# Optimization experiments

Measured on AMD Instinct MI355X. Metric: run time of the kernel, lower is better.

## Reference

```python
import jax, jax.numpy as jnp
import numpy as np

N_NODES = 100000
N_EDGES = 1600000
IN_DIM = 128
OUT_DIM = 128
NEG_SLOPE = 0.2


def setup_inputs() -> dict:
    key = jax.random.key(0)
    ks = jax.random.split(key, 7)
    x = jax.random.normal(ks[0], (N_NODES, IN_DIM), dtype=jnp.float32)
    edge_index = jax.random.randint(ks[1], (2, N_EDGES), 0, N_NODES, dtype=jnp.int32)
    # xavier-ish scale for [in, out] weight layout (y = x @ W)
    s = float(np.sqrt(2.0 / (IN_DIM + OUT_DIM)))
    W_q = jax.random.normal(ks[2], (IN_DIM, OUT_DIM), dtype=jnp.float32) * s
    W_k = jax.random.normal(ks[3], (IN_DIM, OUT_DIM), dtype=jnp.float32) * s
    W_v = jax.random.normal(ks[4], (IN_DIM, OUT_DIM), dtype=jnp.float32) * s
    W_l = jax.random.normal(ks[5], (IN_DIM, OUT_DIM), dtype=jnp.float32) * s
    b_l = jnp.zeros((OUT_DIM,), dtype=jnp.float32)
    return {"x": x, "edge_index": edge_index, "W_q": W_q, "W_k": W_k,
            "W_v": W_v, "W_l": W_l, "b_l": b_l}


def reference(x, edge_index, W_q, W_k, W_v, W_l, b_l):
    num_nodes = x.shape[0]
    row, col = edge_index[0], edge_index[1]

    h_q = x @ W_q                                   # [N, D]
    h_k = x @ W_k                                   # [N, D]
    _h_v = x @ W_v                                  # computed in original, unused downstream

    # aggregated query: sum of neighbor queries per destination node
    q_agg = jax.ops.segment_sum(h_q[col], row, num_segments=num_nodes)  # [N, D]
    k_act = jax.nn.leaky_relu(h_k, NEG_SLOPE)

    # per-edge attention scores (note: original uses raw q_agg, not activated)
    scores = jnp.sum(k_act[row] * q_agg[col], axis=1) / (OUT_DIM ** 0.5)  # [E]

    # scatter-softmax over edges grouped by destination (row)
    max_val = jax.ops.segment_max(scores, row, num_segments=num_nodes)
    exp_scores = jnp.exp(scores - max_val[row])
    sum_exp = jax.ops.segment_sum(exp_scores, row, num_segments=num_nodes)
    alpha = exp_scores / (sum_exp[row] + 1e-8)      # [E]; dropout is identity in eval

    h_proj = x @ W_l + b_l                          # [N, D]
    weighted = alpha[:, None] * h_proj[col]         # [E, D]
    h_prime = jax.ops.segment_sum(weighted, row, num_segments=num_nodes)
    return jax.nn.leaky_relu(h_prime, NEG_SLOPE)
```

## Files before the change

kernel.cpp:

```cpp
#include <hip/hip_runtime.h>
#include <math.h>

#define N_NODES 100000
#define N_EDGES 1600000
#define DIM 128
#define CAP 64

#define NB1 196
#define NPB 512
#define CHUNK1 4096
#define GRID1 391
#define SLOT1 52
#define LSTRIDE 197

typedef short bf16x8 __attribute__((ext_vector_type(8)));
typedef float f32x4 __attribute__((ext_vector_type(4)));

static __device__ __forceinline__ unsigned bf16rne(float f) {
    unsigned u = __float_as_uint(f);
    return (u + 0x7FFFu + ((u >> 16) & 1u)) >> 16;
}
static __device__ __forceinline__ float bflo(unsigned u) { return __uint_as_float(u << 16); }
static __device__ __forceinline__ float bfhi(unsigned u) { return __uint_as_float(u & 0xFFFF0000u); }


__global__ __launch_bounds__(256) void prep_k(
    const float* __restrict__ x, const float* __restrict__ Wq,
    const float* __restrict__ Wk, const float* __restrict__ Wl,
    ushort* __restrict__ xb, ushort* __restrict__ kactb,
    ushort* __restrict__ WqTh, ushort* __restrict__ WqTl,
    ushort* __restrict__ WlTh, ushort* __restrict__ WlTl) {
    __shared__ ushort bh[128 * 136];
    __shared__ ushort blo[128 * 136];
    int t = threadIdx.x;

    if (blockIdx.x < 2) {
        const float* W = (blockIdx.x == 0) ? Wq : Wl;
        ushort* Th = (blockIdx.x == 0) ? WqTh : WlTh;
        ushort* Tl = (blockIdx.x == 0) ? WqTl : WlTl;
        for (int i = t; i < 16384; i += 256) {
            int k = i >> 7, n = i & 127;
            float v = W[i];
            unsigned hi = bf16rne(v);
            float lo = v - bflo(hi);
            Th[n * 128 + k] = (ushort)hi;
            Tl[n * 128 + k] = (ushort)bf16rne(lo);
        }
    }
    for (int i = t; i < 16384; i += 256) {
        int k = i >> 7, n = i & 127;
        float v = Wk[i];
        unsigned hi = bf16rne(v);
        float lo = v - bflo(hi);
        bh[n * 136 + k] = (ushort)hi;
        blo[n * 136 + k] = (ushort)bf16rne(lo);
    }
    __syncthreads();

    int wave = t >> 6, lane = t & 63;
    int ln15 = lane & 15, quad = lane >> 4;
    long base = (long)blockIdx.x * 128 + wave * 32;

    bf16x8 Af[2][4];
#pragma unroll
    for (int r = 0; r < 2; r++) {
        long row = base + r * 16 + ln15;
        long rowc = row < N_NODES ? row : N_NODES - 1;
#pragma unroll
        for (int s = 0; s < 4; s++) {
            int ch = s * 4 + quad;
            const float4* xp = (const float4*)(x + rowc * 128 + ch * 8);
            float4 u0 = xp[0], u1 = xp[1];
            bf16x8 f;
            f[0] = (short)bf16rne(u0.x); f[1] = (short)bf16rne(u0.y);
            f[2] = (short)bf16rne(u0.z); f[3] = (short)bf16rne(u0.w);
            f[4] = (short)bf16rne(u1.x); f[5] = (short)bf16rne(u1.y);
            f[6] = (short)bf16rne(u1.z); f[7] = (short)bf16rne(u1.w);
            Af[r][s] = f;
            if (row < N_NODES) *(bf16x8*)(xb + row * 128 + ch * 8) = f;
        }
    }
    f32x4 acc[2][8];
#pragma unroll
    for (int r = 0; r < 2; r++)
#pragma unroll
        for (int t8 = 0; t8 < 8; t8++) acc[r][t8] = (f32x4){0.f, 0.f, 0.f, 0.f};
#pragma unroll
    for (int phase = 0; phase < 2; phase++) {
        const ushort* B = phase ? blo : bh;
#pragma unroll
        for (int s = 0; s < 4; s++) {
#pragma unroll
            for (int t8 = 0; t8 < 8; t8++) {
                bf16x8 b = *(const bf16x8*)(B + (t8 * 16 + ln15) * 136 + (s * 4 + quad) * 8);
                acc[0][t8] = __builtin_amdgcn_mfma_f32_16x16x32_bf16(Af[0][s], b, acc[0][t8], 0, 0, 0);
                acc[1][t8] = __builtin_amdgcn_mfma_f32_16x16x32_bf16(Af[1][s], b, acc[1][t8], 0, 0, 0);
            }
        }
    }
#pragma unroll
    for (int r = 0; r < 2; r++) {
#pragma unroll
        for (int reg = 0; reg < 4; reg++) {
            long node = base + r * 16 + quad * 4 + reg;
            if (node < N_NODES) {
#pragma unroll
                for (int t8 = 0; t8 < 8; t8++) {
                    float v = acc[r][t8][reg];
                    v = v > 0.f ? v : 0.2f * v;
                    kactb[node * 128 + t8 * 16 + ln15] = (ushort)bf16rne(v);
                }
            }
        }
    }
}


__global__ __launch_bounds__(256) void bin_k(const int* __restrict__ row,
                                             const int* __restrict__ col,
                                             unsigned* __restrict__ bkt,
                                             int* __restrict__ bktc) {
    __shared__ int lcnt[NB1];
    __shared__ unsigned lbuf[SLOT1 * LSTRIDE];
    int t = threadIdx.x, blk = blockIdx.x;
    if (t < NB1) lcnt[t] = 0;
    __syncthreads();
    long base = (long)blk * CHUNK1;
    if (base + CHUNK1 <= N_EDGES) {
        const uint4* r4 = (const uint4*)row + (size_t)blk * 1024;
        const uint4* c4 = (const uint4*)col + (size_t)blk * 1024;
#pragma unroll
        for (int q = 0; q < 4; q++) {
            uint4 rv = r4[q * 256 + t];
            uint4 cv = c4[q * 256 + t];
            unsigned rr[4] = {rv.x, rv.y, rv.z, rv.w};
            unsigned cc[4] = {cv.x, cv.y, cv.z, cv.w};
#pragma unroll
            for (int i = 0; i < 4; i++) {
                int b = rr[i] >> 9;
                int p = atomicAdd(&lcnt[b], 1);
                if (p < SLOT1) lbuf[p * LSTRIDE + b] = (cc[i] << 9) | (rr[i] & 511u);
            }
        }
    } else {
        for (int i = t; base + i < N_EDGES; i += 256) {
            unsigned r = (unsigned)row[base + i], c = (unsigned)col[base + i];
            int b = r >> 9;
            int p = atomicAdd(&lcnt[b], 1);
            if (p < SLOT1) lbuf[p * LSTRIDE + b] = (c << 9) | (r & 511u);
        }
    }
    __syncthreads();
    if (t < NB1) bktc[(size_t)blk * NB1 + t] = min(lcnt[t], SLOT1);
    int wave = t >> 6, lane = t & 63;
    for (int s = wave; s < NB1; s += 4) {
        if (lane < min(lcnt[s], SLOT1))
            bkt[((size_t)s * GRID1 + blk) * SLOT1 + lane] = lbuf[lane * LSTRIDE + s];
    }
}


__global__ __launch_bounds__(1024) void build_k(const int* __restrict__ bktc,
                                                const unsigned* __restrict__ bkt,
                                                int* __restrict__ cur,
                                                int* __restrict__ scol) {
    __shared__ int lcur[NPB];
    __shared__ int lc[GRID1];
    int b = blockIdx.x, t = threadIdx.x;
    if (t < NPB) lcur[t] = 0;
    if (t < GRID1) lc[t] = bktc[(size_t)t * NB1 + b];
    __syncthreads();
    int wave = t >> 6, lane = t & 63;
    const unsigned* D = bkt + (size_t)b * GRID1 * SLOT1;
    for (int s = wave; s < GRID1; s += 16) {
        if (lane < lc[s]) {
            unsigned v = D[(size_t)s * SLOT1 + lane];
            int rl = (int)(v & 511u);
            int c = (int)(v >> 9);
            int p = atomicAdd(&lcur[rl], 1);
            if (p < CAP) scol[((size_t)b * NPB + rl) * CAP + p] = c;
        }
    }
    __syncthreads();
    if (t < NPB) {
        int node = b * NPB + t;
        if (node < N_NODES) cur[node] = lcur[t];
    }
}


__global__ __launch_bounds__(1024) void xq_k(const uint4* __restrict__ xb4,
                                             const int* __restrict__ cur,
                                             const int* __restrict__ scol,
                                             const ushort* __restrict__ BTh,
                                             const ushort* __restrict__ BTl,
                                             ushort* __restrict__ qb) {
    __shared__ ushort lxa[64][136];
    int t = threadIdx.x;
    int g16 = t >> 4, gl = t & 15;
    long node = (long)blockIdx.x * 64 + g16;
    int d = (node < N_NODES) ? min(cur[node], CAP) : 0;
    float a0 = 0.f, a1 = 0.f, a2 = 0.f, a3 = 0.f;
    float a4 = 0.f, a5 = 0.f, a6 = 0.f, a7 = 0.f;
    for (int j = 0; j < d; j += 16) {
        int cb = (j + gl < d) ? scol[node * CAP + j + gl] : 0;
        int lim = min(16, d - j);
        int k = 0;
        for (; k + 4 <= lim; k += 4) {
            int c0 = __shfl(cb, k, 16),     c1 = __shfl(cb, k + 1, 16);
            int c2 = __shfl(cb, k + 2, 16), c3 = __shfl(cb, k + 3, 16);
            uint4 u0 = xb4[(size_t)c0 * 16 + gl];
            uint4 u1 = xb4[(size_t)c1 * 16 + gl];
            uint4 u2 = xb4[(size_t)c2 * 16 + gl];
            uint4 u3 = xb4[(size_t)c3 * 16 + gl];
            a0 += bflo(u0.x); a1 += bfhi(u0.x); a2 += bflo(u0.y); a3 += bfhi(u0.y);
            a4 += bflo(u0.z); a5 += bfhi(u0.z); a6 += bflo(u0.w); a7 += bfhi(u0.w);
            a0 += bflo(u1.x); a1 += bfhi(u1.x); a2 += bflo(u1.y); a3 += bfhi(u1.y);
            a4 += bflo(u1.z); a5 += bfhi(u1.z); a6 += bflo(u1.w); a7 += bfhi(u1.w);
            a0 += bflo(u2.x); a1 += bfhi(u2.x); a2 += bflo(u2.y); a3 += bfhi(u2.y);
            a4 += bflo(u2.z); a5 += bfhi(u2.z); a6 += bflo(u2.w); a7 += bfhi(u2.w);
            a0 += bflo(u3.x); a1 += bfhi(u3.x); a2 += bflo(u3.y); a3 += bfhi(u3.y);
            a4 += bflo(u3.z); a5 += bfhi(u3.z); a6 += bflo(u3.w); a7 += bfhi(u3.w);
        }
        for (; k < lim; k++) {
            int c = __shfl(cb, k, 16);
            uint4 u = xb4[(size_t)c * 16 + gl];
            a0 += bflo(u.x); a1 += bfhi(u.x); a2 += bflo(u.y); a3 += bfhi(u.y);
            a4 += bflo(u.z); a5 += bfhi(u.z); a6 += bflo(u.w); a7 += bfhi(u.w);
        }
    }
    uint4 o;
    o.x = bf16rne(a0) | (bf16rne(a1) << 16);
    o.y = bf16rne(a2) | (bf16rne(a3) << 16);
    o.z = bf16rne(a4) | (bf16rne(a5) << 16);
    o.w = bf16rne(a6) | (bf16rne(a7) << 16);
    *(uint4*)&lxa[g16][gl * 8] = o;
    __syncthreads();

    int wave = t >> 6, lane = t & 63;
    int ln15 = lane & 15, quad = (lane >> 4) & 3;
    const bf16x8* Bh8 = (const bf16x8*)BTh;
    const bf16x8* Bl8 = (const bf16x8*)BTl;
#pragma unroll
    for (int ti = 0; ti < 2; ti++) {
        int T = wave + ti * 16;
        int rt = T & 3, ct = T >> 2;
        bf16x8 af[4];
#pragma unroll
        for (int s = 0; s < 4; s++)
            af[s] = *(const bf16x8*)&lxa[rt * 16 + ln15][(s * 4 + quad) * 8];
        f32x4 acc = (f32x4){0.f, 0.f, 0.f, 0.f};
#pragma unroll
        for (int phase = 0; phase < 2; phase++) {
            const bf16x8* B8 = phase ? Bl8 : Bh8;
#pragma unroll
            for (int s = 0; s < 4; s++)
                acc = __builtin_amdgcn_mfma_f32_16x16x32_bf16(
                    af[s], B8[(ct * 16 + ln15) * 16 + s * 4 + quad], acc, 0, 0, 0);
        }
#pragma unroll
        for (int reg = 0; reg < 4; reg++) {
            long n2 = (long)blockIdx.x * 64 + rt * 16 + quad * 4 + reg;
            if (n2 < N_NODES) qb[n2 * 128 + ct * 16 + ln15] = (ushort)bf16rne(acc[reg]);
        }
    }
}


__global__ __launch_bounds__(1024) void attf_k(const uint2* __restrict__ kactb2,
                                               const uint2* __restrict__ qb2,
                                               const uint2* __restrict__ xb2,
                                               const int* __restrict__ cur,
                                               const int* __restrict__ scol,
                                               const ushort* __restrict__ BTh,
                                               const ushort* __restrict__ BTl,
                                               const float* __restrict__ bl,
                                               float* __restrict__ out) {
    __shared__ ushort lxw[32][136];
    __shared__ float lsw[32];
    int t = threadIdx.x;
    int n32 = t >> 5, lane = t & 31;
    long g = (long)blockIdx.x * 32 + n32;
    int d = min(cur[g], CAP);
    uint2 ku = kactb2[g * 32 + lane];
    const float scale = 0.08838834764831845f;
    float k0 = bflo(ku.x) * scale, k1 = bfhi(ku.x) * scale;
    float k2 = bflo(ku.y) * scale, k3 = bfhi(ku.y) * scale;

    float S = 0.f;
    float a0 = 0.f, a1 = 0.f, a2 = 0.f, a3 = 0.f;
    for (int j = 0; j < d; j += 32) {
        int cb = (j + lane < d) ? scol[g * CAP + j + lane] : 0;
        int lim = min(32, d - j);
        int k = 0;
        for (; k + 4 <= lim; k += 4) {
            int c0 = __shfl(cb, k, 32),     c1 = __shfl(cb, k + 1, 32);
            int c2 = __shfl(cb, k + 2, 32), c3 = __shfl(cb, k + 3, 32);
            uint2 q0 = qb2[(size_t)c0 * 32 + lane], x0 = xb2[(size_t)c0 * 32 + lane];
            uint2 q1 = qb2[(size_t)c1 * 32 + lane], x1 = xb2[(size_t)c1 * 32 + lane];
            uint2 q2 = qb2[(size_t)c2 * 32 + lane], x2 = xb2[(size_t)c2 * 32 + lane];
            uint2 q3 = qb2[(size_t)c3 * 32 + lane], x3 = xb2[(size_t)c3 * 32 + lane];
            float p0 = k0 * bflo(q0.x) + k1 * bfhi(q0.x) + k2 * bflo(q0.y) + k3 * bfhi(q0.y);
            float p1 = k0 * bflo(q1.x) + k1 * bfhi(q1.x) + k2 * bflo(q1.y) + k3 * bfhi(q1.y);
            float p2 = k0 * bflo(q2.x) + k1 * bfhi(q2.x) + k2 * bflo(q2.y) + k3 * bfhi(q2.y);
            float p3 = k0 * bflo(q3.x) + k1 * bfhi(q3.x) + k2 * bflo(q3.y) + k3 * bfhi(q3.y);
#pragma unroll
            for (int off = 16; off > 0; off >>= 1) {
                p0 += __shfl_xor(p0, off, 32); p1 += __shfl_xor(p1, off, 32);
                p2 += __shfl_xor(p2, off, 32); p3 += __shfl_xor(p3, off, 32);
            }
            float e0 = __expf(p0), e1 = __expf(p1);
            float e2 = __expf(p2), e3 = __expf(p3);
            S += (e0 + e1) + (e2 + e3);
            a0 += e0 * bflo(x0.x) + e1 * bflo(x1.x) + e2 * bflo(x2.x) + e3 * bflo(x3.x);
            a1 += e0 * bfhi(x0.x) + e1 * bfhi(x1.x) + e2 * bfhi(x2.x) + e3 * bfhi(x3.x);
            a2 += e0 * bflo(x0.y) + e1 * bflo(x1.y) + e2 * bflo(x2.y) + e3 * bflo(x3.y);
            a3 += e0 * bfhi(x0.y) + e1 * bfhi(x1.y) + e2 * bfhi(x2.y) + e3 * bfhi(x3.y);
        }
        for (; k < lim; k++) {
            int c = __shfl(cb, k, 32);
            uint2 q = qb2[(size_t)c * 32 + lane], xx = xb2[(size_t)c * 32 + lane];
            float p = k0 * bflo(q.x) + k1 * bfhi(q.x) + k2 * bflo(q.y) + k3 * bfhi(q.y);
#pragma unroll
            for (int off = 16; off > 0; off >>= 1) p += __shfl_xor(p, off, 32);
            float e0 = __expf(p);
            S += e0;
            a0 += e0 * bflo(xx.x);
            a1 += e0 * bfhi(xx.x);
            a2 += e0 * bflo(xx.y);
            a3 += e0 * bfhi(xx.y);
        }
    }
    float inv = 1.f / (S + 1e-8f);
    uint2 o;
    o.x = bf16rne(a0 * inv) | (bf16rne(a1 * inv) << 16);
    o.y = bf16rne(a2 * inv) | (bf16rne(a3 * inv) << 16);
    *(uint2*)&lxw[n32][lane * 4] = o;
    if (lane == 0) lsw[n32] = S * inv;
    __syncthreads();

    int wave = t >> 6, l64 = t & 63;
    int ln15 = l64 & 15, quad = (l64 >> 4) & 3;
    int rt = wave & 1, ct = wave >> 1;
    const bf16x8* Bh8 = (const bf16x8*)BTh;
    const bf16x8* Bl8 = (const bf16x8*)BTl;
    bf16x8 af[4];
#pragma unroll
    for (int s = 0; s < 4; s++)
        af[s] = *(const bf16x8*)&lxw[rt * 16 + ln15][(s * 4 + quad) * 8];
    f32x4 acc = (f32x4){0.f, 0.f, 0.f, 0.f};
#pragma unroll
    for (int phase = 0; phase < 2; phase++) {
        const bf16x8* B8 = phase ? Bl8 : Bh8;
#pragma unroll
        for (int s = 0; s < 4; s++)
            acc = __builtin_amdgcn_mfma_f32_16x16x32_bf16(
                af[s], B8[(ct * 16 + ln15) * 16 + s * 4 + quad], acc, 0, 0, 0);
    }
    float blv = bl[ct * 16 + ln15];
#pragma unroll
    for (int reg = 0; reg < 4; reg++) {
        int rrow = rt * 16 + quad * 4 + reg;
        long node = (long)blockIdx.x * 32 + rrow;
        float v = acc[reg] + lsw[rrow] * blv;
        v = v > 0.f ? v : 0.2f * v;
        out[node * 128 + ct * 16 + ln15] = v;
    }
}


extern "C" void kernel_launch(void* const* d_in, const int* in_sizes, int n_in,
                              void* d_out, int out_size, void* d_ws, size_t ws_size,
                              hipStream_t stream) {
    const float* x  = (const float*)d_in[0];
    const int* row  = (const int*)d_in[1];
    const int* col  = row + N_EDGES;
    const float* Wq = (const float*)d_in[2];
    const float* Wk = (const float*)d_in[3];
    const float* Wl = (const float*)d_in[5];
    const float* bl = (const float*)d_in[6];
    float* out = (float*)d_out;

    ushort* xb    = (ushort*)d_ws;
    ushort* qb    = xb + (size_t)N_NODES * DIM;
    ushort* kactb = qb + (size_t)N_NODES * DIM;
    ushort* wbuf  = kactb + (size_t)N_NODES * DIM;
    ushort* WqTh = wbuf,             *WqTl = wbuf + 16384;
    ushort* WlTh = wbuf + 2 * 16384, *WlTl = wbuf + 3 * 16384;
    int* cur  = (int*)(wbuf + 4 * 16384);
    int* scol = cur + N_NODES;
    unsigned* bkt = (unsigned*)(scol + (size_t)N_NODES * CAP);
    int* bktc = (int*)(bkt + (size_t)NB1 * GRID1 * SLOT1);

    prep_k<<<782, 256, 0, stream>>>(x, Wq, Wk, Wl, xb, kactb,
                                    WqTh, WqTl, WlTh, WlTl);
    bin_k<<<GRID1, 256, 0, stream>>>(row, col, bkt, bktc);
    build_k<<<NB1, 1024, 0, stream>>>(bktc, bkt, cur, scol);
    xq_k<<<(N_NODES + 63) / 64, 1024, 0, stream>>>((const uint4*)xb, cur, scol,
                                                   WqTh, WqTl, qb);
    attf_k<<<N_NODES / 32, 1024, 0, stream>>>((const uint2*)kactb, (const uint2*)qb,
                                              (const uint2*)xb, cur, scol,
                                              WlTh, WlTl, bl, out);
}
```

Measured before the change: 470.3 us.

## Interleave q and x rows into one buffer and shrink attention blocks to 8 nodes

The q-projection kernel now stages its bf16 output in shared memory and writes an interleaved [q|x] row per node, so the attention gather fetches one 16-byte vector per lane instead of two separate 8-byte loads from different buffers. The attention kernel moves from 1024-thread/32-node blocks to 256-thread/8-node blocks, with the output MFMA using padded rows (half zeroed) and each wave covering two column tiles. This aims to halve gather transactions and improve latency hiding and tail balance, at the cost of extra write traffic for the duplicated x, a larger workspace, and wasted MFMA work on padded rows.

```diff
diff --git a/kernel.cpp b/kernel.cpp
--- a/kernel.cpp
+++ b/kernel.cpp
@@ -194,8 +194,9 @@
                                              const int* __restrict__ scol,
                                              const ushort* __restrict__ BTh,
                                              const ushort* __restrict__ BTl,
-                                             ushort* __restrict__ qb) {
+                                             uint4* __restrict__ qx4) {
     __shared__ ushort lxa[64][136];
+    __shared__ ushort lq[64][136];
     int t = threadIdx.x;
     int g16 = t >> 4, gl = t & 15;
     long node = (long)blockIdx.x * 64 + g16;
@@ -259,30 +260,44 @@
                     af[s], B8[(ct * 16 + ln15) * 16 + s * 4 + quad], acc, 0, 0, 0);
         }
 #pragma unroll
-        for (int reg = 0; reg < 4; reg++) {
-            long n2 = (long)blockIdx.x * 64 + rt * 16 + quad * 4 + reg;
-            if (n2 < N_NODES) qb[n2 * 128 + ct * 16 + ln15] = (ushort)bf16rne(acc[reg]);
-        }
-    }
-}
-
-
-__global__ __launch_bounds__(1024) void attf_k(const uint2* __restrict__ kactb2,
-                                               const uint2* __restrict__ qb2,
-                                               const uint2* __restrict__ xb2,
-                                               const int* __restrict__ cur,
-                                               const int* __restrict__ scol,
-                                               const ushort* __restrict__ BTh,
-                                               const ushort* __restrict__ BTl,
-                                               const float* __restrict__ bl,
-                                               float* __restrict__ out) {
-    __shared__ ushort lxw[32][136];
-    __shared__ float lsw[32];
+        for (int reg = 0; reg < 4; reg++)
+            lq[rt * 16 + quad * 4 + reg][ct * 16 + ln15] = (ushort)bf16rne(acc[reg]);
+    }
+    __syncthreads();
+
+    const uint2* xb2 = (const uint2*)xb4;
+#pragma unroll
+    for (int i = 0; i < 2; i++) {
+        int idx = i * 1024 + t;
+        int g = idx >> 5, c = idx & 31;
+        long n2 = (long)blockIdx.x * 64 + g;
+        if (n2 < N_NODES) {
+            uint2 q2 = *(const uint2*)&lq[g][c * 4];
+            uint2 x2 = xb2[n2 * 32 + c];
+            qx4[n2 * 32 + c] = make_uint4(q2.x, q2.y, x2.x, x2.y);
+        }
+    }
+}
+
+
+__global__ __launch_bounds__(256) void attf_k(const uint2* __restrict__ kactb,
+                                              const uint4* __restrict__ qx4,
+                                              const int* __restrict__ cur,
+                                              const int* __restrict__ scol,
+                                              const ushort* __restrict__ BTh,
+                                              const ushort* __restrict__ BTl,
+                                              const float* __restrict__ bl,
+                                              float* __restrict__ out) {
+    __shared__ ushort lxw[16][136];
+    __shared__ float lsw[8];
     int t = threadIdx.x;
-    int n32 = t >> 5, lane = t & 31;
-    long g = (long)blockIdx.x * 32 + n32;
+    uint* lf = (uint*)&lxw[0][0];
+    for (int i = t; i < 544; i += 256) lf[544 + i] = 0u;
+
+    int n8 = t >> 5, lane = t & 31;
+    long g = (long)blockIdx.x * 8 + n8;
     int d = min(cur[g], CAP);
-    uint2 ku = kactb2[g * 32 + lane];
+    uint2 ku = kactb[(size_t)g * 32 + lane];
     const float scale = 0.08838834764831845f;
     float k0 = bflo(ku.x) * scale, k1 = bfhi(ku.x) * scale;
     float k2 = bflo(ku.y) * scale, k3 = bfhi(ku.y) * scale;
@@ -296,14 +311,14 @@
         for (; k + 4 <= lim; k += 4) {
             int c0 = __shfl(cb, k, 32),     c1 = __shfl(cb, k + 1, 32);
             int c2 = __shfl(cb, k + 2, 32), c3 = __shfl(cb, k + 3, 32);
-            uint2 q0 = qb2[(size_t)c0 * 32 + lane], x0 = xb2[(size_t)c0 * 32 + lane];
-            uint2 q1 = qb2[(size_t)c1 * 32 + lane], x1 = xb2[(size_t)c1 * 32 + lane];
-            uint2 q2 = qb2[(size_t)c2 * 32 + lane], x2 = xb2[(size_t)c2 * 32 + lane];
-            uint2 q3 = qb2[(size_t)c3 * 32 + lane], x3 = xb2[(size_t)c3 * 32 + lane];
-            float p0 = k0 * bflo(q0.x) + k1 * bfhi(q0.x) + k2 * bflo(q0.y) + k3 * bfhi(q0.y);
-            float p1 = k0 * bflo(q1.x) + k1 * bfhi(q1.x) + k2 * bflo(q1.y) + k3 * bfhi(q1.y);
-            float p2 = k0 * bflo(q2.x) + k1 * bfhi(q2.x) + k2 * bflo(q2.y) + k3 * bfhi(q2.y);
-            float p3 = k0 * bflo(q3.x) + k1 * bfhi(q3.x) + k2 * bflo(q3.y) + k3 * bfhi(q3.y);
+            uint4 u0 = qx4[(size_t)c0 * 32 + lane];
+            uint4 u1 = qx4[(size_t)c1 * 32 + lane];
+            uint4 u2 = qx4[(size_t)c2 * 32 + lane];
+            uint4 u3 = qx4[(size_t)c3 * 32 + lane];
+            float p0 = k0 * bflo(u0.x) + k1 * bfhi(u0.x) + k2 * bflo(u0.y) + k3 * bfhi(u0.y);
+            float p1 = k0 * bflo(u1.x) + k1 * bfhi(u1.x) + k2 * bflo(u1.y) + k3 * bfhi(u1.y);
+            float p2 = k0 * bflo(u2.x) + k1 * bfhi(u2.x) + k2 * bflo(u2.y) + k3 * bfhi(u2.y);
+            float p3 = k0 * bflo(u3.x) + k1 * bfhi(u3.x) + k2 * bflo(u3.y) + k3 * bfhi(u3.y);
 #pragma unroll
             for (int off = 16; off > 0; off >>= 1) {
                 p0 += __shfl_xor(p0, off, 32); p1 += __shfl_xor(p1, off, 32);
@@ -312,59 +327,64 @@
             float e0 = __expf(p0), e1 = __expf(p1);
             float e2 = __expf(p2), e3 = __expf(p3);
             S += (e0 + e1) + (e2 + e3);
-            a0 += e0 * bflo(x0.x) + e1 * bflo(x1.x) + e2 * bflo(x2.x) + e3 * bflo(x3.x);
-            a1 += e0 * bfhi(x0.x) + e1 * bfhi(x1.x) + e2 * bfhi(x2.x) + e3 * bfhi(x3.x);
-            a2 += e0 * bflo(x0.y) + e1 * bflo(x1.y) + e2 * bflo(x2.y) + e3 * bflo(x3.y);
-            a3 += e0 * bfhi(x0.y) + e1 * bfhi(x1.y) + e2 * bfhi(x2.y) + e3 * bfhi(x3.y);
+            a0 += e0 * bflo(u0.z) + e1 * bflo(u1.z) + e2 * bflo(u2.z) + e3 * bflo(u3.z);
+            a1 += e0 * bfhi(u0.z) + e1 * bfhi(u1.z) + e2 * bfhi(u2.z) + e3 * bfhi(u3.z);
+            a2 += e0 * bflo(u0.w) + e1 * bflo(u1.w) + e2 * bflo(u2.w) + e3 * bflo(u3.w);
+            a3 += e0 * bfhi(u0.w) + e1 * bfhi(u1.w) + e2 * bfhi(u2.w) + e3 * bfhi(u3.w);
         }
         for (; k < lim; k++) {
             int c = __shfl(cb, k, 32);
-            uint2 q = qb2[(size_t)c * 32 + lane], xx = xb2[(size_t)c * 32 + lane];
-            float p = k0 * bflo(q.x) + k1 * bfhi(q.x) + k2 * bflo(q.y) + k3 * bfhi(q.y);
+            uint4 u = qx4[(size_t)c * 32 + lane];
+            float p = k0 * bflo(u.x) + k1 * bfhi(u.x) + k2 * bflo(u.y) + k3 * bfhi(u.y);
 #pragma unroll
             for (int off = 16; off > 0; off >>= 1) p += __shfl_xor(p, off, 32);
             float e0 = __expf(p);
             S += e0;
-            a0 += e0 * bflo(xx.x);
-            a1 += e0 * bfhi(xx.x);
-            a2 += e0 * bflo(xx.y);
-            a3 += e0 * bfhi(xx.y);
+            a0 += e0 * bflo(u.z);
+            a1 += e0 * bfhi(u.z);
+            a2 += e0 * bflo(u.w);
+            a3 += e0 * bfhi(u.w);
         }
     }
     float inv = 1.f / (S + 1e-8f);
     uint2 o;
     o.x = bf16rne(a0 * inv) | (bf16rne(a1 * inv) << 16);
     o.y = bf16rne(a2 * inv) | (bf16rne(a3 * inv) << 16);
-    *(uint2*)&lxw[n32][lane * 4] = o;
-    if (lane == 0) lsw[n32] = S * inv;
+    *(uint2*)&lxw[n8][lane * 4] = o;
+    if (lane == 0) lsw[n8] = S * inv;
     __syncthreads();
 
     int wave = t >> 6, l64 = t & 63;
     int ln15 = l64 & 15, quad = (l64 >> 4) & 3;
-    int rt = wave & 1, ct = wave >> 1;
     const bf16x8* Bh8 = (const bf16x8*)BTh;
     const bf16x8* Bl8 = (const bf16x8*)BTl;
     bf16x8 af[4];
 #pragma unroll
     for (int s = 0; s < 4; s++)
-        af[s] = *(const bf16x8*)&lxw[rt * 16 + ln15][(s * 4 + quad) * 8];
-    f32x4 acc = (f32x4){0.f, 0.f, 0.f, 0.f};
-#pragma unroll
-    for (int phase = 0; phase < 2; phase++) {
-        const bf16x8* B8 = phase ? Bl8 : Bh8;
-#pragma unroll
-        for (int s = 0; s < 4; s++)
-            acc = __builtin_amdgcn_mfma_f32_16x16x32_bf16(
-                af[s], B8[(ct * 16 + ln15) * 16 + s * 4 + quad], acc, 0, 0, 0);
-    }
-    float blv = bl[ct * 16 + ln15];
-#pragma unroll
-    for (int reg = 0; reg < 4; reg++) {
-        int rrow = rt * 16 + quad * 4 + reg;
-        long node = (long)blockIdx.x * 32 + rrow;
-        float v = acc[reg] + lsw[rrow] * blv;
-        v = v > 0.f ? v : 0.2f * v;
-        out[node * 128 + ct * 16 + ln15] = v;
+        af[s] = *(const bf16x8*)&lxw[ln15][(s * 4 + quad) * 8];
+#pragma unroll
+    for (int ti = 0; ti < 2; ti++) {
+        int ct = wave + ti * 4;
+        f32x4 acc = (f32x4){0.f, 0.f, 0.f, 0.f};
+#pragma unroll
+        for (int phase = 0; phase < 2; phase++) {
+            const bf16x8* B8 = phase ? Bl8 : Bh8;
+#pragma unroll
+            for (int s = 0; s < 4; s++)
+                acc = __builtin_amdgcn_mfma_f32_16x16x32_bf16(
+                    af[s], B8[(ct * 16 + ln15) * 16 + s * 4 + quad], acc, 0, 0, 0);
+        }
+        float blv = bl[ct * 16 + ln15];
+#pragma unroll
+        for (int reg = 0; reg < 4; reg++) {
+            int rrow = quad * 4 + reg;
+            if (rrow < 8) {
+                long node2 = (long)blockIdx.x * 8 + rrow;
+                float v = acc[reg] + lsw[rrow] * blv;
+                v = v > 0.f ? v : 0.2f * v;
+                out[node2 * 128 + ct * 16 + ln15] = v;
+            }
+        }
     }
 }
 
@@ -382,8 +402,8 @@
     float* out = (float*)d_out;
 
     ushort* xb    = (ushort*)d_ws;
-    ushort* qb    = xb + (size_t)N_NODES * DIM;
-    ushort* kactb = qb + (size_t)N_NODES * DIM;
+    ushort* qx    = xb + (size_t)N_NODES * DIM;
+    ushort* kactb = qx + (size_t)N_NODES * 256;
     ushort* wbuf  = kactb + (size_t)N_NODES * DIM;
     ushort* WqTh = wbuf,             *WqTl = wbuf + 16384;
     ushort* WlTh = wbuf + 2 * 16384, *WlTl = wbuf + 3 * 16384;
@@ -397,8 +417,7 @@
     bin_k<<<GRID1, 256, 0, stream>>>(row, col, bkt, bktc);
     build_k<<<NB1, 1024, 0, stream>>>(bktc, bkt, cur, scol);
     xq_k<<<(N_NODES + 63) / 64, 1024, 0, stream>>>((const uint4*)xb, cur, scol,
-                                                   WqTh, WqTl, qb);
-    attf_k<<<N_NODES / 32, 1024, 0, stream>>>((const uint2*)kactb, (const uint2*)qb,
-                                              (const uint2*)xb, cur, scol,
-                                              WlTh, WlTl, bl, out);
-}
+                                                   WqTh, WqTl, (uint4*)qx);
+    attf_k<<<N_NODES / 8, 256, 0, stream>>>((const uint2*)kactb, (const uint4*)qx,
+                                            cur, scol, WlTh, WlTl, bl, out);
+}
```

New measurement: 490.2 us. 1.04x slower.
